# Kernel tuning notes

Hardware: AMD Instinct MI355X
Metric: run time of the kernel (lower is better)

## Reference

```python
import jax, jax.numpy as jnp
import numpy as np

B, N, D = 8, 1024, 1024

def setup_inputs() -> dict:
    key = jax.random.key(0)
    k1, k2, k3, k4, k5 = jax.random.split(key, 5)
    x = jax.random.normal(k1, (B, N, D), dtype=jnp.float32)
    y = jax.random.normal(k2, (B, N, D), dtype=jnp.float32)
    adj = jax.random.uniform(k3, (B, N, N), dtype=jnp.float32)
    adj_sumrow = jnp.sum(adj, axis=-1, keepdims=True)  # [B, N, 1], row-sum normalizer
    W = jax.random.normal(k4, (D, D), dtype=jnp.float32) * (1.0 / np.sqrt(D))
    b = jax.random.normal(k5, (D,), dtype=jnp.float32) * 0.02
    return {"x": x, "y": y, "adj": adj, "adj_sumrow": adj_sumrow, "W": W, "b": b}

def reference(x, y, adj, adj_sumrow, W, b):
    # GraphConvolutionCustom: project neighbor features, aggregate via dense adj,
    # normalize by row-sum, add bias and residual input x; then ReLU.
    # Dropout is identity in eval mode (training=False).
    support = jnp.einsum('bnd,de->bne', y, W)          # [B, N, D]
    agg = jnp.matmul(adj, support) / adj_sumrow        # [B, N, D]
    out = jax.nn.relu(agg + b + x)
    return out
```

## Files before the change

kernel.cpp:

```cpp
#include <hip/hip_runtime.h>
#include <hip/hip_bf16.h>
#include <stdint.h>


typedef float  f32x4  __attribute__((ext_vector_type(4)));
typedef __bf16 bf16x8 __attribute__((ext_vector_type(8)));

__device__ __forceinline__ unsigned short f2bf(float f) {
  union { float f; unsigned int u; } c; c.f = f;
  unsigned int u = c.u;
  u += 0x7FFFu + ((u >> 16) & 1u);
  return (unsigned short)(u >> 16);
}

__device__ __forceinline__ void async_cp16(const void* g, void* l) {
  __builtin_amdgcn_global_load_lds(
      (const __attribute__((address_space(1))) unsigned int*)g,
      (__attribute__((address_space(3))) unsigned int*)l, 16, 0, 0);
}

__device__ __forceinline__ void bar() { asm volatile("s_barrier" ::: "memory"); }


__global__ __launch_bounds__(256) void k_prep(
    const float4* __restrict__ y4, const float4* __restrict__ a4,
    ushort4* __restrict__ yb, ushort4* __restrict__ ab,
    const float* __restrict__ W, unsigned short* __restrict__ Wt)
{
  __shared__ float t[64][65];
  const int bid = blockIdx.x;
  if (bid < 16384) {
    const int i = bid * 256 + threadIdx.x;
    const bool isY = i < 2097152;
    const float4 v = isY ? y4[i] : a4[i - 2097152];
    ushort4 p;
    p.x = f2bf(v.x); p.y = f2bf(v.y); p.z = f2bf(v.z); p.w = f2bf(v.w);
    if (isY) yb[i] = p; else ab[i - 2097152] = p;
  } else {
    const int id = bid - 16384;
    const int n0 = (id & 15) * 64, k0 = (id >> 4) * 64;
    const int tx = threadIdx.x & 63, ty = threadIdx.x >> 6;
#pragma unroll
    for (int r = ty; r < 64; r += 4)
      t[r][tx] = W[(size_t)(k0 + r) * 1024 + n0 + tx];
    __syncthreads();
#pragma unroll
    for (int r = ty; r < 64; r += 4)
      Wt[(size_t)(n0 + r) * 1024 + k0 + tx] = f2bf(t[tx][r]);
  }
}


__device__ __forceinline__ void stage512(
    const unsigned short* __restrict__ A,  int sA,
    const unsigned short* __restrict__ Bt, int sB,
    int m0, int n0, int k0,
    unsigned short* la, unsigned short* lb,
    int wave, int rg, int colo)
{
#pragma unroll
  for (int s = 0; s < 2; ++s) {
    const int t = wave * 2 + s;
    async_cp16(A  + (size_t)(m0 + t * 8 + rg) * sA + k0 + colo, la + t * 512);
    async_cp16(Bt + (size_t)(n0 + t * 8 + rg) * sB + k0 + colo, lb + t * 512);
  }
}

__device__ __forceinline__ void compute512(
    const unsigned short* la, const unsigned short* lb,
    f32x4 acc[2][4], int wm, int wn, int quad, int l16)
{
#pragma unroll
  for (int h = 0; h < 2; ++h) {
    bf16x8 af[2], bfr[4];
#pragma unroll
    for (int i = 0; i < 2; ++i) {
      const int r = wm + i * 16 + l16;
      af[i] = *(const bf16x8*)(la + r * 64 + ((h * 4 + quad + r) & 7) * 8);
    }
#pragma unroll
    for (int j = 0; j < 4; ++j) {
      const int r = wn + j * 16 + l16;
      bfr[j] = *(const bf16x8*)(lb + r * 64 + ((h * 4 + quad + r) & 7) * 8);
    }
#pragma unroll
    for (int i = 0; i < 2; ++i)
#pragma unroll
      for (int j = 0; j < 4; ++j)
        acc[i][j] = __builtin_amdgcn_mfma_f32_16x16x32_bf16(af[i], bfr[j], acc[i][j], 0, 0, 0);
  }
}

__device__ __forceinline__ void gemm_quad(
    const unsigned short* __restrict__ A,  int sA,
    const unsigned short* __restrict__ Bt, int sB,
    int m0, int n0, f32x4 acc[2][4], unsigned short* lsm, int tid)
{
  const int lane = tid & 63, wave = tid >> 6;
  const int wm = (wave >> 1) * 32, wn = (wave & 1) * 64;
  const int quad = lane >> 4, l16 = lane & 15;
  const int rg = lane >> 3;
  const int colo = (((lane & 7) - rg) & 7) * 8;

  stage512(A, sA, Bt, sB, m0, n0, 0,   lsm,           lsm + 8192,          wave, rg, colo);
  stage512(A, sA, Bt, sB, m0, n0, 64,  lsm + 16384,   lsm + 16384 + 8192,  wave, rg, colo);
  stage512(A, sA, Bt, sB, m0, n0, 128, lsm + 32768,   lsm + 32768 + 8192,  wave, rg, colo);

#pragma unroll
  for (int k = 0; k < 16; ++k) {
    if (k < 13) {
      unsigned short* base = lsm + ((k + 3) & 3) * 16384;
      stage512(A, sA, Bt, sB, m0, n0, (k + 3) * 64, base, base + 8192, wave, rg, colo);
      asm volatile("s_waitcnt vmcnt(12)" ::: "memory");
    } else if (k == 13) {
      asm volatile("s_waitcnt vmcnt(8)" ::: "memory");
    } else if (k == 14) {
      asm volatile("s_waitcnt vmcnt(4)" ::: "memory");
    } else {
      asm volatile("s_waitcnt vmcnt(0)" ::: "memory");
    }
    bar();
    const unsigned short* cb = lsm + (k & 3) * 16384;
    compute512(cb, cb + 8192, acc, wm, wn, quad, l16);
    bar();
  }
}

__device__ __forceinline__ void zero_acc(f32x4 acc[2][4]) {
#pragma unroll
  for (int i = 0; i < 2; ++i)
#pragma unroll
    for (int j = 0; j < 4; ++j)
#pragma unroll
      for (int r = 0; r < 4; ++r) acc[i][j][r] = 0.0f;
}


__global__ __launch_bounds__(512, 2) void k_gemm1(
    const unsigned short* __restrict__ Wt,
    const unsigned short* __restrict__ Ybf,
    unsigned short* __restrict__ Sup2)
{
  __shared__ __align__(16) unsigned short lsm[65536];
  const int tid = threadIdx.x;
  const int bid = blockIdx.x;
  const int l = ((bid & 7) << 6) | (bid >> 3);
  const int m0 = (l & 7) << 7, n0 = (l >> 3) << 7;

  f32x4 acc[2][4];
  zero_acc(acc);
  gemm_quad(Wt, 1024, Ybf, 1024, m0, n0, acc, lsm, tid);

  const int lane = tid & 63, wave = tid >> 6;
  const int wm = (wave >> 1) * 32, wn = (wave & 1) * 64;
  const int quad = lane >> 4, l16 = lane & 15;
#pragma unroll
  for (int i = 0; i < 2; ++i) {
    const int mb = m0 + wm + i * 16 + quad * 4;
#pragma unroll
    for (int r = 0; r < 4; ++r) {
      unsigned short* row = Sup2 + ((size_t)(mb + r) << 13);
#pragma unroll
      for (int j = 0; j < 4; ++j)
        row[n0 + wn + j * 16 + l16] = f2bf(acc[i][j][r]);
    }
  }
}


__global__ __launch_bounds__(512, 2) void k_gemm2(
    const unsigned short* __restrict__ AdjBf,
    const unsigned short* __restrict__ Sup2,
    const float* __restrict__ x,
    const float* __restrict__ sumrow,
    const float* __restrict__ bias,
    float* __restrict__ out)
{
  __shared__ __align__(16) unsigned short lsm[65536];
  const int tid = threadIdx.x;
  const int bid = blockIdx.x;
  const int l = ((bid & 7) << 6) | (bid >> 3);
  const int b = l >> 6;
  const int m0 = ((l >> 3) & 7) << 7, n0 = (l & 7) << 7;

  f32x4 acc[2][4];
  zero_acc(acc);
  gemm_quad(AdjBf + ((size_t)b << 20), 1024,
            Sup2 + ((size_t)b << 10), 8192,
            m0, n0, acc, lsm, tid);

  const float* xb = x   + ((size_t)b << 20);
  float*       ob = out + ((size_t)b << 20);
  const float* sr = sumrow + ((size_t)b << 10);
  const int lane = tid & 63, wave = tid >> 6;
  const int wm = (wave >> 1) * 32, wn = (wave & 1) * 64;
  const int quad = lane >> 4, l16 = lane & 15;

  float bv[4];
#pragma unroll
  for (int j = 0; j < 4; ++j) bv[j] = bias[n0 + wn + j * 16 + l16];

#pragma unroll
  for (int i = 0; i < 2; ++i) {
    const int mb = m0 + wm + i * 16 + quad * 4;
#pragma unroll
    for (int r = 0; r < 4; ++r) {
      const int m = mb + r;
      const float inv = 1.0f / sr[m];
#pragma unroll
      for (int j = 0; j < 4; ++j) {
        const int n = n0 + wn + j * 16 + l16;
        const size_t idx = (((size_t)m) << 10) + n;
        float v = acc[i][j][r] * inv + bv[j] + xb[idx];
        ob[idx] = fmaxf(v, 0.0f);
      }
    }
  }
}


extern "C" void kernel_launch(void* const* d_in, const int* in_sizes, int n_in,
                              void* d_out, int out_size, void* d_ws, size_t ws_size,
                              hipStream_t stream) {
  const float* x      = (const float*)d_in[0];
  const float* y      = (const float*)d_in[1];
  const float* adj    = (const float*)d_in[2];
  const float* sumrow = (const float*)d_in[3];
  const float* W      = (const float*)d_in[4];
  const float* bias   = (const float*)d_in[5];
  float* out = (float*)d_out;

  char* ws = (char*)d_ws;
  unsigned short* ybf   = (unsigned short*)(ws);
  unsigned short* adjbf = (unsigned short*)(ws + ((size_t)16 << 20));
  unsigned short* wt    = (unsigned short*)(ws + ((size_t)32 << 20));
  unsigned short* sup2  = (unsigned short*)(ws + ((size_t)34 << 20));

  k_prep<<<dim3(16640), dim3(256), 0, stream>>>(
      (const float4*)y, (const float4*)adj, (ushort4*)ybf, (ushort4*)adjbf, W, wt);
  k_gemm1<<<dim3(512), dim3(512), 0, stream>>>(wt, ybf, sup2);
  k_gemm2<<<dim3(512), dim3(512), 0, stream>>>(adjbf, sup2, x, sumrow, bias, out);
}
```

Baseline: 198.3 us.

## Enlarge GEMM tiles to 256x256 with double-buffered interleaved staging pipeline

Both GEMM kernels move from 128x128 block tiles to 256x256 tiles, with each of the 8 waves computing a 128x64 sub-tile. The K loop becomes a two-stage LDS double buffer in which A and B halves are staged in quarter pieces, interleaved with the MFMA clusters. Those clusters run under raised wave priority. Block-to-tile mapping is reworked per XCD and the grids shrink from 512 to 128 blocks. The goal is more operand reuse and less global/LDS traffic per FLOP, at the cost of fewer blocks than CUs and higher register pressure.

```diff
diff --git a/kernel.cpp b/kernel.cpp
--- a/kernel.cpp
+++ b/kernel.cpp
@@ -20,6 +20,7 @@
 }
 
 __device__ __forceinline__ void bar() { asm volatile("s_barrier" ::: "memory"); }
+#define VMCNT(n) asm volatile("s_waitcnt vmcnt(" #n ")" ::: "memory")
 
 
 __global__ __launch_bounds__(256) void k_prep(
@@ -51,84 +52,137 @@
 }
 
 
-__device__ __forceinline__ void stage512(
+__device__ __forceinline__ void stageA(
+    const unsigned short* __restrict__ A, int sA, int m0, int k0, int c,
+    unsigned short* la, int wave, int rg, int colo)
+{
+#pragma unroll
+  for (int s = 0; s < 2; ++s) {
+    const int t = wave * 2 + s;
+    const int row0 = (t >> 3) * 128 + c * 64 + (t & 7) * 8;
+    async_cp16(A + (size_t)(m0 + row0 + rg) * sA + k0 + colo, la + row0 * 64);
+  }
+}
+
+__device__ __forceinline__ void stageB(
+    const unsigned short* __restrict__ Bt, int sB, int n0, int k0, int c,
+    unsigned short* lb, int wave, int rg, int colo)
+{
+#pragma unroll
+  for (int s = 0; s < 2; ++s) {
+    const int t = wave * 2 + s;
+    const int row0 = (t >> 2) * 64 + c * 32 + (t & 3) * 8;
+    async_cp16(Bt + (size_t)(n0 + row0 + rg) * sB + k0 + colo, lb + row0 * 64);
+  }
+}
+
+__device__ __forceinline__ void readA(
+    const unsigned short* la, bf16x8 af[2][4], int wm, int mh, int quad, int l16)
+{
+#pragma unroll
+  for (int h = 0; h < 2; ++h)
+#pragma unroll
+    for (int i = 0; i < 4; ++i) {
+      const int r = wm + mh * 64 + i * 16 + l16;
+      af[h][i] = *(const bf16x8*)(la + r * 64 + ((h * 4 + quad + r) & 7) * 8);
+    }
+}
+
+__device__ __forceinline__ void readB(
+    const unsigned short* lb, bf16x8 bfr[2][2], int wn, int nh, int quad, int l16)
+{
+#pragma unroll
+  for (int h = 0; h < 2; ++h)
+#pragma unroll
+    for (int j = 0; j < 2; ++j) {
+      const int r = wn + nh * 32 + j * 16 + l16;
+      bfr[h][j] = *(const bf16x8*)(lb + r * 64 + ((h * 4 + quad + r) & 7) * 8);
+    }
+}
+
+__device__ __forceinline__ void quad16(
+    bf16x8 af[2][4], bf16x8 bfr[2][2], f32x4 acc[8][4], int mh, int nh)
+{
+  __builtin_amdgcn_s_setprio(1);
+#pragma unroll
+  for (int h = 0; h < 2; ++h)
+#pragma unroll
+    for (int i = 0; i < 4; ++i)
+#pragma unroll
+      for (int j = 0; j < 2; ++j)
+        acc[mh * 4 + i][nh * 2 + j] = __builtin_amdgcn_mfma_f32_16x16x32_bf16(
+            af[h][i], bfr[h][j], acc[mh * 4 + i][nh * 2 + j], 0, 0, 0);
+  __builtin_amdgcn_s_setprio(0);
+}
+
+__device__ __forceinline__ void gemm256(
     const unsigned short* __restrict__ A,  int sA,
     const unsigned short* __restrict__ Bt, int sB,
-    int m0, int n0, int k0,
-    unsigned short* la, unsigned short* lb,
-    int wave, int rg, int colo)
-{
-#pragma unroll
-  for (int s = 0; s < 2; ++s) {
-    const int t = wave * 2 + s;
-    async_cp16(A  + (size_t)(m0 + t * 8 + rg) * sA + k0 + colo, la + t * 512);
-    async_cp16(Bt + (size_t)(n0 + t * 8 + rg) * sB + k0 + colo, lb + t * 512);
-  }
-}
-
-__device__ __forceinline__ void compute512(
-    const unsigned short* la, const unsigned short* lb,
-    f32x4 acc[2][4], int wm, int wn, int quad, int l16)
-{
-#pragma unroll
-  for (int h = 0; h < 2; ++h) {
-    bf16x8 af[2], bfr[4];
-#pragma unroll
-    for (int i = 0; i < 2; ++i) {
-      const int r = wm + i * 16 + l16;
-      af[i] = *(const bf16x8*)(la + r * 64 + ((h * 4 + quad + r) & 7) * 8);
-    }
-#pragma unroll
-    for (int j = 0; j < 4; ++j) {
-      const int r = wn + j * 16 + l16;
-      bfr[j] = *(const bf16x8*)(lb + r * 64 + ((h * 4 + quad + r) & 7) * 8);
-    }
-#pragma unroll
-    for (int i = 0; i < 2; ++i)
-#pragma unroll
-      for (int j = 0; j < 4; ++j)
-        acc[i][j] = __builtin_amdgcn_mfma_f32_16x16x32_bf16(af[i], bfr[j], acc[i][j], 0, 0, 0);
-  }
-}
-
-__device__ __forceinline__ void gemm_quad(
-    const unsigned short* __restrict__ A,  int sA,
-    const unsigned short* __restrict__ Bt, int sB,
-    int m0, int n0, f32x4 acc[2][4], unsigned short* lsm, int tid)
+    int m0, int n0, f32x4 acc[8][4], unsigned short* lsm, int tid)
 {
   const int lane = tid & 63, wave = tid >> 6;
-  const int wm = (wave >> 1) * 32, wn = (wave & 1) * 64;
+  const int wm = (wave >> 2) * 128, wn = (wave & 3) * 64;
   const int quad = lane >> 4, l16 = lane & 15;
   const int rg = lane >> 3;
   const int colo = (((lane & 7) - rg) & 7) * 8;
 
-  stage512(A, sA, Bt, sB, m0, n0, 0,   lsm,           lsm + 8192,          wave, rg, colo);
-  stage512(A, sA, Bt, sB, m0, n0, 64,  lsm + 16384,   lsm + 16384 + 8192,  wave, rg, colo);
-  stage512(A, sA, Bt, sB, m0, n0, 128, lsm + 32768,   lsm + 32768 + 8192,  wave, rg, colo);
-
-#pragma unroll
-  for (int k = 0; k < 16; ++k) {
-    if (k < 13) {
-      unsigned short* base = lsm + ((k + 3) & 3) * 16384;
-      stage512(A, sA, Bt, sB, m0, n0, (k + 3) * 64, base, base + 8192, wave, rg, colo);
-      asm volatile("s_waitcnt vmcnt(12)" ::: "memory");
-    } else if (k == 13) {
-      asm volatile("s_waitcnt vmcnt(8)" ::: "memory");
-    } else if (k == 14) {
-      asm volatile("s_waitcnt vmcnt(4)" ::: "memory");
-    } else {
-      asm volatile("s_waitcnt vmcnt(0)" ::: "memory");
-    }
-    bar();
-    const unsigned short* cb = lsm + (k & 3) * 16384;
-    compute512(cb, cb + 8192, acc, wm, wn, quad, l16);
-    bar();
-  }
-}
-
-__device__ __forceinline__ void zero_acc(f32x4 acc[2][4]) {
-#pragma unroll
-  for (int i = 0; i < 2; ++i)
+  bf16x8 af[2][4], bfr[2][2];
+
+  stageA(A, sA, m0, 0, 0, lsm,        wave, rg, colo);
+  stageB(Bt, sB, n0, 0, 0, lsm + 16384, wave, rg, colo);
+  stageB(Bt, sB, n0, 0, 1, lsm + 16384, wave, rg, colo);
+  stageA(A, sA, m0, 0, 1, lsm,        wave, rg, colo);
+
+#pragma unroll 1
+  for (int T = 0; T < 15; ++T) {
+    const unsigned short* la = lsm + (T & 1) * 32768;
+    const unsigned short* lb = la + 16384;
+    unsigned short* na = lsm + ((T + 1) & 1) * 32768;
+    unsigned short* nb = na + 16384;
+    const int nk = (T + 1) * 64;
+
+    VMCNT(4); bar();
+    stageA(A, sA, m0, nk, 0, na, wave, rg, colo);
+    readA(la, af, wm, 0, quad, l16);
+    readB(lb, bfr, wn, 0, quad, l16);
+    quad16(af, bfr, acc, 0, 0);
+
+    VMCNT(4); bar();
+    stageB(Bt, sB, n0, nk, 0, nb, wave, rg, colo);
+    readB(lb, bfr, wn, 1, quad, l16);
+    quad16(af, bfr, acc, 0, 1);
+
+    VMCNT(4); bar();
+    stageB(Bt, sB, n0, nk, 1, nb, wave, rg, colo);
+    readA(la, af, wm, 1, quad, l16);
+    quad16(af, bfr, acc, 1, 1);
+
+    stageA(A, sA, m0, nk, 1, na, wave, rg, colo);
+    readB(lb, bfr, wn, 0, quad, l16);
+    quad16(af, bfr, acc, 1, 0);
+  }
+
+  {
+    const unsigned short* la = lsm + 32768;
+    const unsigned short* lb = la + 16384;
+    VMCNT(4); bar();
+    readA(la, af, wm, 0, quad, l16);
+    readB(lb, bfr, wn, 0, quad, l16);
+    quad16(af, bfr, acc, 0, 0);
+    VMCNT(2); bar();
+    readB(lb, bfr, wn, 1, quad, l16);
+    quad16(af, bfr, acc, 0, 1);
+    VMCNT(0); bar();
+    readA(la, af, wm, 1, quad, l16);
+    quad16(af, bfr, acc, 1, 1);
+    readB(lb, bfr, wn, 0, quad, l16);
+    quad16(af, bfr, acc, 1, 0);
+  }
+}
+
+__device__ __forceinline__ void zero_acc(f32x4 acc[8][4]) {
+#pragma unroll
+  for (int i = 0; i < 8; ++i)
 #pragma unroll
     for (int j = 0; j < 4; ++j)
 #pragma unroll
@@ -143,26 +197,26 @@
 {
   __shared__ __align__(16) unsigned short lsm[65536];
   const int tid = threadIdx.x;
-  const int bid = blockIdx.x;
-  const int l = ((bid & 7) << 6) | (bid >> 3);
-  const int m0 = (l & 7) << 7, n0 = (l >> 3) << 7;
-
-  f32x4 acc[2][4];
+  const int xcd = blockIdx.x & 7, slot = blockIdx.x >> 3;
+  const int m0 = (slot >> 2) * 256;
+  const int n0 = (xcd * 4 + (slot & 3)) * 256;
+
+  f32x4 acc[8][4];
   zero_acc(acc);
-  gemm_quad(Wt, 1024, Ybf, 1024, m0, n0, acc, lsm, tid);
+  gemm256(Wt, 1024, Ybf, 1024, m0, n0, acc, lsm, tid);
 
   const int lane = tid & 63, wave = tid >> 6;
-  const int wm = (wave >> 1) * 32, wn = (wave & 1) * 64;
+  const int wm = (wave >> 2) * 128, wn = (wave & 3) * 64;
   const int quad = lane >> 4, l16 = lane & 15;
 #pragma unroll
-  for (int i = 0; i < 2; ++i) {
-    const int mb = m0 + wm + i * 16 + quad * 4;
+  for (int mi = 0; mi < 8; ++mi) {
+    const int mb = m0 + wm + mi * 16 + quad * 4;
 #pragma unroll
     for (int r = 0; r < 4; ++r) {
       unsigned short* row = Sup2 + ((size_t)(mb + r) << 13);
 #pragma unroll
-      for (int j = 0; j < 4; ++j)
-        row[n0 + wn + j * 16 + l16] = f2bf(acc[i][j][r]);
+      for (int nj = 0; nj < 4; ++nj)
+        row[n0 + wn + nj * 16 + l16] = f2bf(acc[mi][nj][r]);
     }
   }
 }
@@ -178,40 +232,38 @@
 {
   __shared__ __align__(16) unsigned short lsm[65536];
   const int tid = threadIdx.x;
-  const int bid = blockIdx.x;
-  const int l = ((bid & 7) << 6) | (bid >> 3);
-  const int b = l >> 6;
-  const int m0 = ((l >> 3) & 7) << 7, n0 = (l & 7) << 7;
-
-  f32x4 acc[2][4];
+  const int b = blockIdx.x & 7, slot = blockIdx.x >> 3;
+  const int m0 = (slot >> 2) * 256, n0 = (slot & 3) * 256;
+
+  f32x4 acc[8][4];
   zero_acc(acc);
-  gemm_quad(AdjBf + ((size_t)b << 20), 1024,
-            Sup2 + ((size_t)b << 10), 8192,
-            m0, n0, acc, lsm, tid);
+  gemm256(AdjBf + ((size_t)b << 20), 1024,
+          Sup2 + ((size_t)b << 10), 8192,
+          m0, n0, acc, lsm, tid);
 
   const float* xb = x   + ((size_t)b << 20);
   float*       ob = out + ((size_t)b << 20);
   const float* sr = sumrow + ((size_t)b << 10);
   const int lane = tid & 63, wave = tid >> 6;
-  const int wm = (wave >> 1) * 32, wn = (wave & 1) * 64;
+  const int wm = (wave >> 2) * 128, wn = (wave & 3) * 64;
   const int quad = lane >> 4, l16 = lane & 15;
 
   float bv[4];
 #pragma unroll
-  for (int j = 0; j < 4; ++j) bv[j] = bias[n0 + wn + j * 16 + l16];
-
-#pragma unroll
-  for (int i = 0; i < 2; ++i) {
-    const int mb = m0 + wm + i * 16 + quad * 4;
+  for (int nj = 0; nj < 4; ++nj) bv[nj] = bias[n0 + wn + nj * 16 + l16];
+
+#pragma unroll
+  for (int mi = 0; mi < 8; ++mi) {
+    const int mb = m0 + wm + mi * 16 + quad * 4;
 #pragma unroll
     for (int r = 0; r < 4; ++r) {
       const int m = mb + r;
       const float inv = 1.0f / sr[m];
 #pragma unroll
-      for (int j = 0; j < 4; ++j) {
-        const int n = n0 + wn + j * 16 + l16;
+      for (int nj = 0; nj < 4; ++nj) {
+        const int n = n0 + wn + nj * 16 + l16;
         const size_t idx = (((size_t)m) << 10) + n;
-        float v = acc[i][j][r] * inv + bv[j] + xb[idx];
+        float v = acc[mi][nj][r] * inv + bv[nj] + xb[idx];
         ob[idx] = fmaxf(v, 0.0f);
       }
     }
@@ -238,6 +290,6 @@
 
   k_prep<<<dim3(16640), dim3(256), 0, stream>>>(
       (const float4*)y, (const float4*)adj, (ushort4*)ybf, (ushort4*)adjbf, W, wt);
-  k_gemm1<<<dim3(512), dim3(512), 0, stream>>>(wt, ybf, sup2);
-  k_gemm2<<<dim3(512), dim3(512), 0, stream>>>(adjbf, sup2, x, sumrow, bias, out);
-}
+  k_gemm1<<<dim3(128), dim3(512), 0, stream>>>(wt, ybf, sup2);
+  k_gemm2<<<dim3(128), dim3(512), 0, stream>>>(adjbf, sup2, x, sumrow, bias, out);
+}
```

Result: slower. 223.8 us (+12.9%).
